# Kernel optimization log

Measured on AMD Instinct MI355X. Metric: run time of the kernel, lower is better.

The kernel has to match this reference:

```python
import jax, jax.numpy as jnp
import numpy as np

B, D, E, H, O, K = 8192, 3072, 8, 2048, 512, 2
EPS = float(np.finfo(float).eps)  # np.finfo(float).eps used in SparseDispatcher.combine


def _cv_squared(v):
    # torch .var() is unbiased (ddof=1)
    v = v.astype(jnp.float32)
    return jnp.var(v, ddof=1) / (jnp.mean(v) ** 2 + 1e-10)


def setup_inputs() -> dict:
    key = jax.random.key(0)
    ks = jax.random.split(key, 8)
    x = jax.random.normal(ks[0], (B, D), dtype=jnp.float32)
    Cats = jax.random.uniform(ks[1], (B, E), dtype=jnp.float32)
    w_gate = jax.random.normal(ks[2], (D, E), dtype=jnp.float32) * 0.01
    # per-expert 2-layer MLP standing in for the per-expert ResNet
    W1 = jax.random.normal(ks[3], (E, D, H), dtype=jnp.float32) * (1.0 / np.sqrt(D))
    b1 = jnp.zeros((E, H), dtype=jnp.float32)
    W2 = jax.random.normal(ks[4], (E, H, O), dtype=jnp.float32) * (1.0 / np.sqrt(H))
    b2 = jnp.zeros((E, O), dtype=jnp.float32)
    return {"x": x, "Cats": Cats, "w_gate": w_gate, "W1": W1, "b1": b1,
            "W2": W2, "b2": b2, "train": 0}


def reference(x, Cats, w_gate, W1, b1, W2, b2, train):
    # ---- top_k_gating (eval path; train branch mutates optimizer state) ----
    logits = x @ w_gate                                   # [B, E]
    top_vals, top_idx = jax.lax.top_k(logits, min(K + 1, E))
    top_k_vals = top_vals[:, :K]                          # [B, K]
    top_k_idx = top_idx[:, :K]                            # [B, K]
    top_k_gates = jax.nn.softmax(top_k_vals, axis=1)      # softmax over kept logits
    rows = jnp.arange(x.shape[0])[:, None]
    gates = jnp.zeros_like(logits).at[rows, top_k_idx].set(top_k_gates)  # scatter

    load = (gates > 0).sum(axis=0)                        # tokens per expert
    importance = gates.sum(axis=0)
    aux_loss = 0.01 * (_cv_squared(importance) + _cv_squared(load))

    # ---- dispatch / expert / combine ----
    # Dense grouped form: expert_i runs on its routed tokens; tokens with
    # gates[b,i]==0 contribute exactly 0 to the combine, identical math to
    # SparseDispatcher's gather/split + exp*gate + index_add + log.
    h = jax.nn.relu(jnp.einsum('bd,edh->beh', x, W1) + b1[None])  # [B, E, H]
    out = jnp.einsum('beh,eho->beo', h, W2) + b2[None]            # [B, E, O]
    combined = jnp.einsum('be,beo->bo', gates, jnp.exp(out))      # exp, *gate, sum
    combined = jnp.where(combined == 0, EPS, combined)
    y = jnp.log(combined)
    return (y, aux_loss)
```

## Files before the change

kernel.cpp:

```cpp
#include <hip/hip_runtime.h>
#include <stdint.h>


typedef __bf16 bf16x8 __attribute__((ext_vector_type(8)));
typedef __bf16 bf16x4 __attribute__((ext_vector_type(4)));
typedef float floatx4 __attribute__((ext_vector_type(4)));

#define EPSF 2.2204460492503131e-16f

__device__ __forceinline__ void gl_lds16(const void* g, void* l) {
  __builtin_amdgcn_global_load_lds(
      (__attribute__((address_space(1))) void*)(g),
      (__attribute__((address_space(3))) void*)(l), 16, 0, 0);
}

__global__ __launch_bounds__(512) void k_gating(
    const float* __restrict__ x, const float* __restrict__ wg,
    __bf16* __restrict__ x_bf, int* __restrict__ expsel,
    float* __restrict__ gpair) {
  __shared__ float wgs[12320];
  const int tid = threadIdx.x;
  const int lane = tid & 63;
  const int w = tid >> 6;
  const int r = blockIdx.x * 8 + w;
  const int g = lane >> 3;
  const int e = lane & 7;
  const float* xr = x + (size_t)r * 3072;
  __bf16* xbr = x_bf + (size_t)r * 3072;

#pragma unroll
  for (int t = 0; t < 12; ++t) {
    const int d = t * 256 + lane * 4;
    const float4 xv = *(const float4*)(xr + d);
    bf16x4 xo;
    xo.x = (__bf16)xv.x; xo.y = (__bf16)xv.y;
    xo.z = (__bf16)xv.z; xo.w = (__bf16)xv.w;
    *(bf16x4*)(xbr + d) = xo;
  }

  double a0 = 0.0, a1 = 0.0;
  for (int h = 0; h < 2; ++h) {
    __syncthreads();
#pragma unroll
    for (int t = 0; t < 6; ++t) {
      const int wi = t * 2048 + tid * 4;
      const int gg = wi / 1536;
      const float4 v = *(const float4*)(wg + h * 12288 + wi);
      *(float4*)(wgs + wi + 4 * gg) = v;
    }
    __syncthreads();
    const float* xrg = xr + h * 1536 + g * 192;
    const float* wbase = wgs + g * 1540 + e;
    for (int i = 0; i < 192; i += 4) {
      const float4 xv = *(const float4*)(xrg + i);
      a0 += (double)xv.x * (double)wbase[(i + 0) * 8];
      a1 += (double)xv.y * (double)wbase[(i + 1) * 8];
      a0 += (double)xv.z * (double)wbase[(i + 2) * 8];
      a1 += (double)xv.w * (double)wbase[(i + 3) * 8];
    }
  }
  double v = a0 + a1;
  v += __shfl_xor(v, 8);
  v += __shfl_xor(v, 16);
  v += __shfl_xor(v, 32);
  double le[8];
#pragma unroll
  for (int ee = 0; ee < 8; ++ee) le[ee] = __shfl(v, ee);
  if (lane == 0) {
    int i0 = 0; double v0 = le[0];
#pragma unroll
    for (int k = 1; k < 8; ++k) if (le[k] > v0) { v0 = le[k]; i0 = k; }
    int i1 = (i0 == 0) ? 1 : 0; double v1 = le[i1];
#pragma unroll
    for (int k = 0; k < 8; ++k)
      if (k != i0 && le[k] > v1 && k != i1) { v1 = le[k]; i1 = k; }
    const float tt = (float)exp(v1 - v0);
    const float g0 = 1.0f / (1.0f + tt);
    const float g1 = tt / (1.0f + tt);
    expsel[r] = i0 | (i1 << 4);
    gpair[r * 2] = g0;
    gpair[r * 2 + 1] = g1;
  }
}

__global__ __launch_bounds__(256) void k_build_lists(
    const int* __restrict__ expsel, const float* __restrict__ gpair,
    int* __restrict__ lists, int* __restrict__ cnt, double* __restrict__ imp) {
  const int e = blockIdx.x;
  const int tid = threadIdx.x;
  const int lane = tid & 63;
  const int w = tid >> 6;
  __shared__ int wsum[4];
  __shared__ double dsum[4];
  int base = 0;
  double gsum = 0.0;
  int* out = lists + e * 8192;
  for (int c = 0; c < 32; ++c) {
    const int r = c * 256 + tid;
    const int sel = expsel[r];
    const bool m0 = ((sel & 15) == e);
    const bool m1 = (((sel >> 4) & 15) == e);
    const bool m = m0 || m1;
    const int entry = 2 * r + (m1 ? 1 : 0);
    const unsigned long long mask = __ballot(m);
    const int wcount = __popcll(mask);
    const int pos = __popcll(mask & ((1ull << lane) - 1ull));
    if (lane == 0) wsum[w] = wcount;
    __syncthreads();
    int pre = base;
#pragma unroll
    for (int ww = 0; ww < 4; ++ww) if (ww < w) pre += wsum[ww];
    const int total = wsum[0] + wsum[1] + wsum[2] + wsum[3];
    if (m) {
      out[pre + pos] = entry;
      gsum += (double)gpair[entry];
    }
    base += total;
    __syncthreads();
  }
  gsum += __shfl_down(gsum, 32);
  gsum += __shfl_down(gsum, 16);
  gsum += __shfl_down(gsum, 8);
  gsum += __shfl_down(gsum, 4);
  gsum += __shfl_down(gsum, 2);
  gsum += __shfl_down(gsum, 1);
  if (lane == 0) dsum[w] = gsum;
  __syncthreads();
  if (tid == 0) {
    imp[e] = dsum[0] + dsum[1] + dsum[2] + dsum[3];
    cnt[e] = base;
  }
}

__global__ void k_sched_aux(const int* __restrict__ cnt, const double* __restrict__ imp,
                            int* __restrict__ sched, int* __restrict__ nslots,
                            int* __restrict__ sched2, int* __restrict__ nslots2,
                            float* __restrict__ aux_out) {
  if (threadIdx.x != 0 || blockIdx.x != 0) return;
  int ns = 0, ns2 = 0;
  for (int e = 0; e < 8; ++e) {
    const int c = cnt[e];
    const int t = (c + 127) >> 7;
    for (int i = 0; i < t; ++i) { sched[2 * ns] = e; sched[2 * ns + 1] = i << 7; ++ns; }
    const int t2 = (c + 255) >> 8;
    for (int i = 0; i < t2; ++i) { sched2[2 * ns2] = e; sched2[2 * ns2 + 1] = i << 8; ++ns2; }
  }
  *nslots = ns;
  *nslots2 = ns2;
  double mi = 0.0, ml = 0.0;
  for (int e = 0; e < 8; ++e) { mi += imp[e]; ml += (double)cnt[e]; }
  mi *= 0.125; ml *= 0.125;
  double vi = 0.0, vl = 0.0;
  for (int e = 0; e < 8; ++e) {
    const double di = imp[e] - mi; vi += di * di;
    const double dl = (double)cnt[e] - ml; vl += dl * dl;
  }
  vi /= 7.0; vl /= 7.0;
  aux_out[0] = (float)(0.01 * (vi / (mi * mi + 1e-10) + vl / (ml * ml + 1e-10)));
}

__global__ __launch_bounds__(256) void k_transpose_cvt(
    const float* __restrict__ in, __bf16* __restrict__ out, int R, int C) {
  __shared__ float tile[64][65];
  const int e = blockIdx.z;
  const int c0 = blockIdx.x * 64;
  const int r0 = blockIdx.y * 64;
  const float* src = in + (size_t)e * R * C + (size_t)r0 * C + c0;
  __bf16* dst = out + (size_t)e * R * C + (size_t)c0 * R + r0;
  const int tx = threadIdx.x & 15;
  const int ty = threadIdx.x >> 4;
#pragma unroll
  for (int i = 0; i < 4; ++i) {
    const int row = ty + i * 16;
    const float4 v = *(const float4*)(src + (size_t)row * C + tx * 4);
    tile[row][tx * 4 + 0] = v.x;
    tile[row][tx * 4 + 1] = v.y;
    tile[row][tx * 4 + 2] = v.z;
    tile[row][tx * 4 + 3] = v.w;
  }
  __syncthreads();
#pragma unroll
  for (int i = 0; i < 4; ++i) {
    const int cc = ty + i * 16;
    const int rr = tx * 4;
    bf16x4 o;
    o.x = (__bf16)tile[rr + 0][cc];
    o.y = (__bf16)tile[rr + 1][cc];
    o.z = (__bf16)tile[rr + 2][cc];
    o.w = (__bf16)tile[rr + 3][cc];
    *(bf16x4*)(dst + (size_t)cc * R + rr) = o;
  }
}

template <int KDIM>
__global__ __launch_bounds__(512, 2) void k_moe_gemm256(
    const __bf16* __restrict__ Asrc, const __bf16* __restrict__ Ball,
    const float* __restrict__ bias, const int* __restrict__ lists,
    const int* __restrict__ cnt, const int* __restrict__ sched,
    const int* __restrict__ nslots, __bf16* __restrict__ hout) {
  constexpr int NT = KDIM / 64;
  __shared__ __bf16 lds2[2 * 24576];

  const int nwg = gridDim.x * gridDim.y;
  int lin = blockIdx.y * gridDim.x + blockIdx.x;
  const int q = nwg >> 3, r = nwg & 7;
  const int xcd = lin & 7, idx = lin >> 3;
  lin = (xcd < r) ? (xcd * (q + 1) + idx) : (r * (q + 1) + (xcd - r) * q + idx);
  const int slot = lin >> 4;
  const int ntile = lin & 15;
  if (slot >= *nslots) return;

  const int e = sched[2 * slot];
  const int row0 = sched[2 * slot + 1];
  const int cnte = cnt[e];
  if (cnte <= 0) return;
  const int n0 = ntile * 128;

  const int tid = threadIdx.x;
  const int lane = tid & 63;
  const int w = __builtin_amdgcn_readfirstlane(tid >> 6);
  const int wm = w >> 1;
  const int wn = w & 1;
  const int lr = lane >> 3;
  const int kc = (lane & 7) ^ lr;

  const __bf16* Be = Ball + (size_t)e * 2048 * KDIM;
  const int* liste = lists + e * 8192;

  const __bf16* aptr[4];
#pragma unroll
  for (int j = 0; j < 4; ++j) {
    int m = row0 + w * 32 + j * 8 + lr;
    m = (m < cnte) ? m : (cnte - 1);
    aptr[j] = Asrc + (size_t)(liste[m] >> 1) * KDIM + kc * 8;
  }
  const __bf16* bptr[2];
#pragma unroll
  for (int j = 0; j < 2; ++j)
    bptr[j] = Be + (size_t)(n0 + w * 16 + j * 8 + lr) * KDIM + kc * 8;

  floatx4 acc[4][4];
#pragma unroll
  for (int i = 0; i < 4; ++i)
#pragma unroll
    for (int j = 0; j < 4; ++j) {
      acc[i][j].x = 0.f; acc[i][j].y = 0.f; acc[i][j].z = 0.f; acc[i][j].w = 0.f;
    }

  auto STAGE = [&](int buf, int kt) {
    __bf16* base = lds2 + buf * 24576;
    const int ko = kt * 64;
#pragma unroll
    for (int j = 0; j < 4; ++j)
      gl_lds16(aptr[j] + ko, base + (w * 32 + j * 8) * 64);
#pragma unroll
    for (int j = 0; j < 2; ++j)
      gl_lds16(bptr[j] + ko, base + 16384 + (w * 16 + j * 8) * 64);
  };

  STAGE(0, 0);

  const int frow = lane & 15;
  const int fr7 = lane & 7;
  const int fch = lane >> 4;
  const int axo0 = ((fch) ^ fr7) * 8;
  const int axo1 = ((4 + fch) ^ fr7) * 8;

  for (int kt = 0; kt < NT; ++kt) {
    __syncthreads();
    if (kt + 1 < NT) STAGE((kt + 1) & 1, kt + 1);
    const __bf16* Abuf = lds2 + (kt & 1) * 24576;
    const __bf16* Bbuf = Abuf + 16384;
    bf16x8 bfr[2][4];
#pragma unroll
    for (int j = 0; j < 4; ++j) {
      const __bf16* brow = Bbuf + (wn * 64 + j * 16 + frow) * 64;
      bfr[0][j] = *(const bf16x8*)(brow + axo0);
      bfr[1][j] = *(const bf16x8*)(brow + axo1);
    }
#pragma unroll
    for (int i = 0; i < 4; ++i) {
      const __bf16* arow = Abuf + (wm * 64 + i * 16 + frow) * 64;
      const bf16x8 a0 = *(const bf16x8*)(arow + axo0);
      const bf16x8 a1 = *(const bf16x8*)(arow + axo1);
#pragma unroll
      for (int j = 0; j < 4; ++j) {
        acc[i][j] = __builtin_amdgcn_mfma_f32_16x16x32_bf16(a0, bfr[0][j], acc[i][j], 0, 0, 0);
        acc[i][j] = __builtin_amdgcn_mfma_f32_16x16x32_bf16(a1, bfr[1][j], acc[i][j], 0, 0, 0);
      }
    }
  }

  const int cq = lane >> 4;
  const int cn = lane & 15;
#pragma unroll
  for (int i = 0; i < 4; ++i) {
#pragma unroll
    for (int rr = 0; rr < 4; ++rr) {
      const int m = row0 + wm * 64 + i * 16 + cq * 4 + rr;
      if (m < cnte) {
        const int p = liste[m];
        __bf16* orow = hout + (size_t)p * 2048;
#pragma unroll
        for (int j = 0; j < 4; ++j) {
          const int n = n0 + wn * 64 + j * 16 + cn;
          float v = acc[i][j][rr] + bias[e * 2048 + n];
          orow[n] = (__bf16)(v > 0.0f ? v : 0.0f);
        }
      }
    }
  }
}

template <int KDIM, int MODE>
__global__ __launch_bounds__(256, 2) void k_moe_gemm(
    const __bf16* __restrict__ Asrc, const __bf16* __restrict__ Ball,
    const float* __restrict__ bias, const int* __restrict__ lists,
    const int* __restrict__ cnt, const int* __restrict__ sched,
    const int* __restrict__ nslots, const float* __restrict__ gpair,
    __bf16* __restrict__ hout, float* __restrict__ oout) {
  constexpr int NDIM = (MODE == 0) ? 2048 : 512;
  const int slot = blockIdx.y;
  if (slot >= *nslots) return;
  const int e = sched[2 * slot];
  const int row0 = sched[2 * slot + 1];
  const int cnte = cnt[e];
  if (cnte <= 0) return;
  const int n0 = blockIdx.x * 128;

  __shared__ unsigned short As[128 * 32];
  __shared__ unsigned short Bs[128 * 32];

  const int tid = threadIdx.x;
  const int lane = tid & 63;
  const int wid = __builtin_amdgcn_readfirstlane(tid >> 6);
  const int wm = wid >> 1;
  const int wn = wid & 1;

  const __bf16* Be = Ball + (size_t)e * NDIM * KDIM;
  const int* liste = lists + e * 8192;
  const int acol = (lane & 3) * 8;

  const __bf16* aptr[2];
  const __bf16* bptr[2];
#pragma unroll
  for (int p = 0; p < 2; ++p) {
    const int chunk = wid + 4 * p;
    const int lr = chunk * 16 + (lane >> 2);
    int m = row0 + lr;
    m = (m < cnte) ? m : (cnte - 1);
    const int entry = liste[m];
    const int srow = (MODE == 0) ? (entry >> 1) : entry;
    aptr[p] = Asrc + (size_t)srow * KDIM + acol;
    bptr[p] = Be + (size_t)(n0 + lr) * KDIM + acol;
  }

  floatx4 acc[4][4];
#pragma unroll
  for (int i = 0; i < 4; ++i)
#pragma unroll
    for (int j = 0; j < 4; ++j) {
      acc[i][j].x = 0.f; acc[i][j].y = 0.f; acc[i][j].z = 0.f; acc[i][j].w = 0.f;
    }

  for (int k0 = 0; k0 < KDIM; k0 += 32) {
#pragma unroll
    for (int p = 0; p < 2; ++p) {
      gl_lds16(aptr[p] + k0, &As[(wid + 4 * p) * 512]);
      gl_lds16(bptr[p] + k0, &Bs[(wid + 4 * p) * 512]);
    }
    __syncthreads();
    bf16x8 af[4], bfr[4];
    const int rdoff = (lane & 15) * 32 + (lane >> 4) * 8;
#pragma unroll
    for (int i = 0; i < 4; ++i)
      af[i] = *(const bf16x8*)&As[(wm * 64 + i * 16) * 32 + rdoff];
#pragma unroll
    for (int j = 0; j < 4; ++j)
      bfr[j] = *(const bf16x8*)&Bs[(wn * 64 + j * 16) * 32 + rdoff];
    __syncthreads();
#pragma unroll
    for (int i = 0; i < 4; ++i)
#pragma unroll
      for (int j = 0; j < 4; ++j)
        acc[i][j] = __builtin_amdgcn_mfma_f32_16x16x32_bf16(af[i], bfr[j], acc[i][j], 0, 0, 0);
  }

  const int cq = lane >> 4;
  const int cn = lane & 15;
#pragma unroll
  for (int i = 0; i < 4; ++i) {
#pragma unroll
    for (int r = 0; r < 4; ++r) {
      const int m = row0 + wm * 64 + i * 16 + cq * 4 + r;
      if (m < cnte) {
        const int p = liste[m];
        if (MODE == 0) {
          __bf16* orow = hout + (size_t)p * 2048;
#pragma unroll
          for (int j = 0; j < 4; ++j) {
            const int n = n0 + wn * 64 + j * 16 + cn;
            float v = acc[i][j][r] + bias[e * 2048 + n];
            v = v > 0.0f ? v : 0.0f;
            orow[n] = (__bf16)v;
          }
        } else {
          float* orow = oout + (size_t)p * 512;
          const float g = gpair[p];
#pragma unroll
          for (int j = 0; j < 4; ++j) {
            const int n = n0 + wn * 64 + j * 16 + cn;
            const float v = acc[i][j][r] + bias[e * 512 + n];
            orow[n] = g * __expf(v);
          }
        }
      }
    }
  }
}

__global__ __launch_bounds__(128) void k_combine(const float* __restrict__ op,
                                                 float* __restrict__ y) {
  const int r = blockIdx.x;
  const int o = threadIdx.x * 4;
  const float4 a = *(const float4*)(op + (size_t)(2 * r) * 512 + o);
  const float4 b = *(const float4*)(op + (size_t)(2 * r + 1) * 512 + o);
  float4 res;
  float s;
  s = a.x + b.x; if (s == 0.0f) s = EPSF; res.x = logf(s);
  s = a.y + b.y; if (s == 0.0f) s = EPSF; res.y = logf(s);
  s = a.z + b.z; if (s == 0.0f) s = EPSF; res.z = logf(s);
  s = a.w + b.w; if (s == 0.0f) s = EPSF; res.w = logf(s);
  *(float4*)(y + (size_t)r * 512 + o) = res;
}

extern "C" void kernel_launch(void* const* d_in, const int* in_sizes, int n_in,
                              void* d_out, int out_size, void* d_ws, size_t ws_size,
                              hipStream_t stream) {
  (void)in_sizes; (void)n_in; (void)out_size; (void)ws_size;
  const float* x  = (const float*)d_in[0];
  const float* wg = (const float*)d_in[2];
  const float* W1 = (const float*)d_in[3];
  const float* b1 = (const float*)d_in[4];
  const float* W2 = (const float*)d_in[5];
  const float* b2 = (const float*)d_in[6];
  float* y = (float*)d_out;

  char* w = (char*)d_ws;
  __bf16* x_bf = (__bf16*)w; w += (size_t)8192 * 3072 * 2;
  __bf16* w1t  = (__bf16*)w; w += (size_t)8 * 2048 * 3072 * 2;
  __bf16* w2t  = (__bf16*)w; w += (size_t)8 * 512 * 2048 * 2;
  __bf16* hp   = (__bf16*)w; w += (size_t)16384 * 2048 * 2;
  float*  op   = (float*)w;  w += (size_t)16384 * 512 * 4;
  int*    lists= (int*)w;    w += (size_t)8 * 8192 * 4;
  float*  gpr  = (float*)w;  w += (size_t)16384 * 4;
  int*    expsel=(int*)w;    w += (size_t)8192 * 4;
  int*    cnt  = (int*)w;    w += 64;
  double* imp  = (double*)w; w += 64;
  int*    sched= (int*)w;    w += 2 * 136 * 4;
  int*    nslots=(int*)w;    w += 64;
  int*    sched2=(int*)w;    w += 2 * 72 * 4;
  int*    nslots2=(int*)w;   w += 64;

  hipLaunchKernelGGL(k_gating, dim3(1024), dim3(512), 0, stream, x, wg, x_bf, expsel, gpr);
  hipLaunchKernelGGL(k_build_lists, dim3(8), dim3(256), 0, stream, expsel, gpr, lists, cnt, imp);
  hipLaunchKernelGGL(k_transpose_cvt, dim3(32, 48, 8), dim3(256), 0, stream, W1, w1t, 3072, 2048);
  hipLaunchKernelGGL(k_transpose_cvt, dim3(8, 32, 8), dim3(256), 0, stream, W2, w2t, 2048, 512);
  hipLaunchKernelGGL(k_sched_aux, dim3(1), dim3(64), 0, stream, cnt, imp, sched, nslots,
                     sched2, nslots2, y + (size_t)8192 * 512);
  hipLaunchKernelGGL((k_moe_gemm256<3072>), dim3(16, 72), dim3(512), 0, stream,
                     x_bf, w1t, b1, lists, cnt, sched2, nslots2, hp);
  hipLaunchKernelGGL((k_moe_gemm<2048, 1>), dim3(4, 136), dim3(256), 0, stream,
                     hp, w2t, b2, lists, cnt, sched, nslots, gpr,
                     (__bf16*)nullptr, op);
  hipLaunchKernelGGL(k_combine, dim3(8192), dim3(128), 0, stream, op, y);
}
```

Measured before the change: 808.8 us.

## Enlarge first expert GEMM tile to 256x256 with barrier-interleaved staging

The first expert GEMM moves from 256x128 output tiles to 256x256 tiles, with 8 waves arranged 2x4 and 128 accumulators per lane. The K loop is split into four quarter phases, each issuing part of the next tile's global-to-LDS loads and then a block of MFMAs. Phases are separated by explicit barriers, partial vmcnt waits and setprio. The aim is more operand reuse per byte loaded and loads overlapping compute, at the cost of higher register and LDS pressure (128KB LDS) and possibly lower occupancy.

```diff
diff --git a/kernel.cpp b/kernel.cpp
--- a/kernel.cpp
+++ b/kernel.cpp
@@ -199,105 +199,166 @@
     const int* __restrict__ cnt, const int* __restrict__ sched,
     const int* __restrict__ nslots, __bf16* __restrict__ hout) {
   constexpr int NT = KDIM / 64;
-  __shared__ __bf16 lds2[2 * 24576];
+  __shared__ __bf16 lds[2 * 32768];
 
   const int nwg = gridDim.x * gridDim.y;
   int lin = blockIdx.y * gridDim.x + blockIdx.x;
-  const int q = nwg >> 3, r = nwg & 7;
-  const int xcd = lin & 7, idx = lin >> 3;
-  lin = (xcd < r) ? (xcd * (q + 1) + idx) : (r * (q + 1) + (xcd - r) * q + idx);
-  const int slot = lin >> 4;
-  const int ntile = lin & 15;
+  const int q = nwg >> 3, rr8 = nwg & 7;
+  const int xcd = lin & 7, bidx = lin >> 3;
+  lin = (xcd < rr8) ? (xcd * (q + 1) + bidx) : (rr8 * (q + 1) + (xcd - rr8) * q + bidx);
+  const int slot = lin >> 3;
+  const int ntile = lin & 7;
   if (slot >= *nslots) return;
 
   const int e = sched[2 * slot];
   const int row0 = sched[2 * slot + 1];
   const int cnte = cnt[e];
   if (cnte <= 0) return;
-  const int n0 = ntile * 128;
+  const int n0 = ntile * 256;
 
   const int tid = threadIdx.x;
   const int lane = tid & 63;
   const int w = __builtin_amdgcn_readfirstlane(tid >> 6);
-  const int wm = w >> 1;
-  const int wn = w & 1;
-  const int lr = lane >> 3;
-  const int kc = (lane & 7) ^ lr;
-
+  const int wm = w >> 2;
+  const int wn = w & 3;
+
+  const int* liste = lists + e * 8192;
   const __bf16* Be = Ball + (size_t)e * 2048 * KDIM;
-  const int* liste = lists + e * 8192;
-
-  const __bf16* aptr[4];
-#pragma unroll
-  for (int j = 0; j < 4; ++j) {
-    int m = row0 + w * 32 + j * 8 + lr;
-    m = (m < cnte) ? m : (cnte - 1);
-    aptr[j] = Asrc + (size_t)(liste[m] >> 1) * KDIM + kc * 8;
-  }
-  const __bf16* bptr[2];
-#pragma unroll
-  for (int j = 0; j < 2; ++j)
-    bptr[j] = Be + (size_t)(n0 + w * 16 + j * 8 + lr) * KDIM + kc * 8;
-
-  floatx4 acc[4][4];
-#pragma unroll
-  for (int i = 0; i < 4; ++i)
+
+  const int rt0 = tid >> 2;
+  const int rt1 = 128 + rt0;
+  const __bf16* agrow[2];
+  const __bf16* bgrow[2];
+  {
+    int m0 = row0 + rt0; m0 = (m0 < cnte) ? m0 : (cnte - 1);
+    int m1 = row0 + rt1; m1 = (m1 < cnte) ? m1 : (cnte - 1);
+    agrow[0] = Asrc + (size_t)(liste[m0] >> 1) * KDIM;
+    agrow[1] = Asrc + (size_t)(liste[m1] >> 1) * KDIM;
+    bgrow[0] = Be + (size_t)(n0 + rt0) * KDIM;
+    bgrow[1] = Be + (size_t)(n0 + rt1) * KDIM;
+  }
+  const int csw = ((tid & 3) ^ ((rt0 >> 1) & 3)) * 8;
+  const int wdst = w * 512;
+
+  auto STAGE = [&](int buf, int kt, int isB, int s) {
+    const int ko = kt * 64 + s * 32 + csw;
+    const int dbase = buf * 32768 + isB * 16384 + s * 8192 + wdst;
+    gl_lds16((isB ? bgrow[0] : agrow[0]) + ko, lds + dbase);
+    gl_lds16((isB ? bgrow[1] : agrow[1]) + ko, lds + dbase + 4096);
+  };
+
+  const int frow = lane & 15;
+  const int fch = lane >> 4;
+  const int rsw = (frow >> 1) & 3;
+  const int aRd = (wm * 128 + frow) * 32 + (fch ^ rsw) * 8;
+  const int bRd = 16384 + (wn * 64 + frow) * 32 + (fch ^ rsw) * 8;
+
+  floatx4 acc[8][4];
+#pragma unroll
+  for (int i = 0; i < 8; ++i)
 #pragma unroll
     for (int j = 0; j < 4; ++j) {
       acc[i][j].x = 0.f; acc[i][j].y = 0.f; acc[i][j].z = 0.f; acc[i][j].w = 0.f;
     }
 
-  auto STAGE = [&](int buf, int kt) {
-    __bf16* base = lds2 + buf * 24576;
-    const int ko = kt * 64;
-#pragma unroll
-    for (int j = 0; j < 4; ++j)
-      gl_lds16(aptr[j] + ko, base + (w * 32 + j * 8) * 64);
-#pragma unroll
-    for (int j = 0; j < 2; ++j)
-      gl_lds16(bptr[j] + ko, base + 16384 + (w * 16 + j * 8) * 64);
-  };
-
-  STAGE(0, 0);
-
-  const int frow = lane & 15;
-  const int fr7 = lane & 7;
-  const int fch = lane >> 4;
-  const int axo0 = ((fch) ^ fr7) * 8;
-  const int axo1 = ((4 + fch) ^ fr7) * 8;
-
+  STAGE(0, 0, 0, 0);
+  STAGE(0, 0, 1, 0);
+  STAGE(0, 0, 0, 1);
+  STAGE(0, 0, 1, 1);
+  asm volatile("s_waitcnt vmcnt(4)" ::: "memory");
+  __builtin_amdgcn_s_barrier();
+  __builtin_amdgcn_sched_barrier(0);
+
+  bf16x8 bf[4];
   for (int kt = 0; kt < NT; ++kt) {
-    __syncthreads();
-    if (kt + 1 < NT) STAGE((kt + 1) & 1, kt + 1);
-    const __bf16* Abuf = lds2 + (kt & 1) * 24576;
-    const __bf16* Bbuf = Abuf + 16384;
-    bf16x8 bfr[2][4];
-#pragma unroll
-    for (int j = 0; j < 4; ++j) {
-      const __bf16* brow = Bbuf + (wn * 64 + j * 16 + frow) * 64;
-      bfr[0][j] = *(const bf16x8*)(brow + axo0);
-      bfr[1][j] = *(const bf16x8*)(brow + axo1);
-    }
-#pragma unroll
-    for (int i = 0; i < 4; ++i) {
-      const __bf16* arow = Abuf + (wm * 64 + i * 16 + frow) * 64;
-      const bf16x8 a0 = *(const bf16x8*)(arow + axo0);
-      const bf16x8 a1 = *(const bf16x8*)(arow + axo1);
-#pragma unroll
-      for (int j = 0; j < 4; ++j) {
-        acc[i][j] = __builtin_amdgcn_mfma_f32_16x16x32_bf16(a0, bfr[0][j], acc[i][j], 0, 0, 0);
-        acc[i][j] = __builtin_amdgcn_mfma_f32_16x16x32_bf16(a1, bfr[1][j], acc[i][j], 0, 0, 0);
-      }
+    const int cur = kt & 1, nxt = cur ^ 1;
+    const __bf16* Ab = lds + cur * 32768;
+    const bool st = (kt + 1 < NT);
+
+    {
+      bf16x8 af[4];
+#pragma unroll
+      for (int i = 0; i < 4; ++i) af[i] = *(const bf16x8*)(Ab + aRd + i * 512);
+#pragma unroll
+      for (int j = 0; j < 4; ++j) bf[j] = *(const bf16x8*)(Ab + bRd + j * 512);
+      if (st) STAGE(nxt, kt + 1, 0, 0);
+      __builtin_amdgcn_s_barrier();
+      __builtin_amdgcn_sched_barrier(0);
+      __builtin_amdgcn_s_setprio(1);
+#pragma unroll
+      for (int i = 0; i < 4; ++i)
+#pragma unroll
+        for (int j = 0; j < 4; ++j)
+          acc[i][j] = __builtin_amdgcn_mfma_f32_16x16x32_bf16(af[i], bf[j], acc[i][j], 0, 0, 0);
+      __builtin_amdgcn_s_setprio(0);
+      __builtin_amdgcn_s_barrier();
+      __builtin_amdgcn_sched_barrier(0);
+    }
+    {
+      bf16x8 af[4];
+#pragma unroll
+      for (int i = 0; i < 4; ++i) af[i] = *(const bf16x8*)(Ab + aRd + (4 + i) * 512);
+      if (st) STAGE(nxt, kt + 1, 1, 0);
+      __builtin_amdgcn_s_barrier();
+      __builtin_amdgcn_sched_barrier(0);
+      __builtin_amdgcn_s_setprio(1);
+#pragma unroll
+      for (int i = 0; i < 4; ++i)
+#pragma unroll
+        for (int j = 0; j < 4; ++j)
+          acc[4 + i][j] = __builtin_amdgcn_mfma_f32_16x16x32_bf16(af[i], bf[j], acc[4 + i][j], 0, 0, 0);
+      __builtin_amdgcn_s_setprio(0);
+      if (st) { asm volatile("s_waitcnt vmcnt(4)" ::: "memory"); }
+      else    { asm volatile("s_waitcnt vmcnt(0)" ::: "memory"); }
+      __builtin_amdgcn_s_barrier();
+      __builtin_amdgcn_sched_barrier(0);
+    }
+    {
+      bf16x8 af[4];
+#pragma unroll
+      for (int i = 0; i < 4; ++i) af[i] = *(const bf16x8*)(Ab + 8192 + aRd + (4 + i) * 512);
+#pragma unroll
+      for (int j = 0; j < 4; ++j) bf[j] = *(const bf16x8*)(Ab + 8192 + bRd + j * 512);
+      if (st) STAGE(nxt, kt + 1, 0, 1);
+      __builtin_amdgcn_s_barrier();
+      __builtin_amdgcn_sched_barrier(0);
+      __builtin_amdgcn_s_setprio(1);
+#pragma unroll
+      for (int i = 0; i < 4; ++i)
+#pragma unroll
+        for (int j = 0; j < 4; ++j)
+          acc[4 + i][j] = __builtin_amdgcn_mfma_f32_16x16x32_bf16(af[i], bf[j], acc[4 + i][j], 0, 0, 0);
+      __builtin_amdgcn_s_setprio(0);
+      __builtin_amdgcn_s_barrier();
+      __builtin_amdgcn_sched_barrier(0);
+    }
+    {
+      bf16x8 af[4];
+#pragma unroll
+      for (int i = 0; i < 4; ++i) af[i] = *(const bf16x8*)(Ab + 8192 + aRd + i * 512);
+      if (st) STAGE(nxt, kt + 1, 1, 1);
+      __builtin_amdgcn_s_barrier();
+      __builtin_amdgcn_sched_barrier(0);
+      __builtin_amdgcn_s_setprio(1);
+#pragma unroll
+      for (int i = 0; i < 4; ++i)
+#pragma unroll
+        for (int j = 0; j < 4; ++j)
+          acc[i][j] = __builtin_amdgcn_mfma_f32_16x16x32_bf16(af[i], bf[j], acc[i][j], 0, 0, 0);
+      __builtin_amdgcn_s_setprio(0);
+      asm volatile("s_waitcnt vmcnt(4)" ::: "memory");
+      __builtin_amdgcn_s_barrier();
+      __builtin_amdgcn_sched_barrier(0);
     }
   }
 
   const int cq = lane >> 4;
   const int cn = lane & 15;
 #pragma unroll
-  for (int i = 0; i < 4; ++i) {
+  for (int i = 0; i < 8; ++i) {
 #pragma unroll
     for (int rr = 0; rr < 4; ++rr) {
-      const int m = row0 + wm * 64 + i * 16 + cq * 4 + rr;
+      const int m = row0 + wm * 128 + i * 16 + cq * 4 + rr;
       if (m < cnte) {
         const int p = liste[m];
         __bf16* orow = hout + (size_t)p * 2048;
@@ -468,7 +529,7 @@
   hipLaunchKernelGGL(k_transpose_cvt, dim3(8, 32, 8), dim3(256), 0, stream, W2, w2t, 2048, 512);
   hipLaunchKernelGGL(k_sched_aux, dim3(1), dim3(64), 0, stream, cnt, imp, sched, nslots,
                      sched2, nslots2, y + (size_t)8192 * 512);
-  hipLaunchKernelGGL((k_moe_gemm256<3072>), dim3(16, 72), dim3(512), 0, stream,
+  hipLaunchKernelGGL((k_moe_gemm256<3072>), dim3(8, 72), dim3(512), 0, stream,
                      x_bf, w1t, b1, lists, cnt, sched2, nslots2, hp);
   hipLaunchKernelGGL((k_moe_gemm<2048, 1>), dim3(4, 136), dim3(256), 0, stream,
                      hp, w2t, b2, lists, cnt, sched, nslots, gpr,
```

Result: faster. 772.5 us (-4.5%).
